# Kernel tuning notes

Hardware: AMD Instinct MI355X
Metric: run time of the kernel (lower is better)

The kernel has to match this reference:

```python
import jax, jax.numpy as jnp
import numpy as np

H = 1024       # hidden_size
VOCAB = 32000  # output_size
L = 128        # max_length
B = 64         # batch


def setup_inputs() -> dict:
    key = jax.random.key(0)
    ks = jax.random.split(key, 16)
    inp = {
        "input_ids": jax.random.randint(ks[0], (1, B), 0, VOCAB),
        "hidden": jax.random.normal(ks[1], (1, B, H), jnp.float32),
        "encoder_outputs": jax.random.normal(ks[2], (L, B, H), jnp.float32),
        # parameters
        "emb": jax.random.normal(ks[3], (VOCAB, H), jnp.float32) * 0.02,
        "attn_W": jax.random.normal(ks[4], (H, 2 * H), jnp.float32) * 0.02,
        "attn_b": jnp.zeros((H,), jnp.float32),
        "v": jax.random.uniform(ks[5], (H,), jnp.float32),
        "w_ih": jax.random.normal(ks[6], (3 * H, 2 * H), jnp.float32) * 0.02,
        "w_hh": jax.random.normal(ks[7], (3 * H, H), jnp.float32) * 0.02,
        "b_ih": jnp.zeros((3 * H,), jnp.float32),
        "b_hh": jnp.zeros((3 * H,), jnp.float32),
        "out_W": jax.random.normal(ks[8], (VOCAB, 3 * H), jnp.float32) * 0.02,
        "out_b": jnp.zeros((VOCAB,), jnp.float32),
    }
    return inp


def reference(input_ids, hidden, encoder_outputs, emb, attn_W, attn_b, v,
              w_ih, w_hh, b_ih, b_hh, out_W, out_b):
    # Dropout in eval mode (identity).
    embedded = emb[input_ids]                      # [1, B, H]
    eo = jnp.transpose(encoder_outputs, (1, 0, 2))  # [B, L, H]
    h0 = hidden[0]                                  # [B, H]

    # Additive (Bahdanau) attention score
    h_rep = jnp.broadcast_to(h0[:, None, :], (eo.shape[0], eo.shape[1], h0.shape[-1]))
    cat = jnp.concatenate([eo, h_rep], axis=-1)     # [B, L, 2H]
    energy = jnp.tanh(jnp.einsum('blk,hk->blh', cat, attn_W) + attn_b)  # [B, L, H]
    scores = jnp.einsum('blh,h->bl', energy, v)     # [B, L]
    attention = jax.nn.softmax(scores, axis=-1)     # [B, L]
    weighted = jnp.einsum('bl,blh->bh', attention, eo)  # [B, H]

    # GRU cell (single layer, single timestep), PyTorch gate order r,z,n
    x = jnp.concatenate([embedded[0], weighted], axis=-1)  # [B, 2H]
    gx = x @ w_ih.T + b_ih                                  # [B, 3H]
    gh = h0 @ w_hh.T + b_hh                                 # [B, 3H]
    xr, xz, xn = jnp.split(gx, 3, axis=-1)
    hr, hz, hn = jnp.split(gh, 3, axis=-1)
    r = jax.nn.sigmoid(xr + hr)
    z = jax.nn.sigmoid(xz + hz)
    n = jnp.tanh(xn + r * hn)
    h_new = (1.0 - z) * n + z * h0                          # [B, H]

    out_cat = jnp.concatenate([h_new, weighted, embedded[0]], axis=-1)  # [B, 3H]
    output = out_cat @ out_W.T + out_b                      # [B, VOCAB]
    return output, h_new[None], attention[:, None, :]
```

## Files before the change

### kernel.cpp

```cpp
#include <hip/hip_runtime.h>
#include <math.h>

#define Hdim 1024
#define VOC 32000
#define LSEQ 128
#define BSZ 64

typedef __attribute__((ext_vector_type(8))) short bf16x8;
typedef __attribute__((ext_vector_type(4))) float f32x4;

__device__ __forceinline__ float fast_tanhf(float x) {
    return 1.0f - 2.0f / (__expf(2.0f * x) + 1.0f);
}
__device__ __forceinline__ float sigmoidf(float x) {
    return 1.0f / (1.0f + __expf(-x));
}
__device__ __forceinline__ short f2bf(float f) {
    unsigned u = __float_as_uint(f);
    unsigned r = (u + 0x7fffu + ((u >> 16) & 1u)) >> 16;
    return (short)r;
}

__device__ __forceinline__ void stage16(const float* __restrict__ src, short* dst) {
    f32x4 v0 = *(const f32x4*)(src);
    f32x4 v1 = *(const f32x4*)(src + 4);
    f32x4 v2 = *(const f32x4*)(src + 8);
    f32x4 v3 = *(const f32x4*)(src + 12);
    bf16x8 p0, p1;
    p0[0] = f2bf(v0[0]); p0[1] = f2bf(v0[1]); p0[2] = f2bf(v0[2]); p0[3] = f2bf(v0[3]);
    p0[4] = f2bf(v1[0]); p0[5] = f2bf(v1[1]); p0[6] = f2bf(v1[2]); p0[7] = f2bf(v1[3]);
    p1[0] = f2bf(v2[0]); p1[1] = f2bf(v2[1]); p1[2] = f2bf(v2[2]); p1[3] = f2bf(v2[3]);
    p1[4] = f2bf(v3[0]); p1[5] = f2bf(v3[1]); p1[6] = f2bf(v3[2]); p1[7] = f2bf(v3[3]);
    *(bf16x8*)(dst) = p0;
    *(bf16x8*)(dst + 8) = p1;
}

__global__ __launch_bounds__(256) void convert_bf16(
    const float* __restrict__ enc, const float* __restrict__ attnW,
    const float* __restrict__ hidden,
    short* __restrict__ enc_bf, short* __restrict__ attnW_bf,
    short* __restrict__ hidden_bf)
{
    const int NG_ENC = (LSEQ * BSZ * Hdim) / 8;
    const int NG_AW  = (Hdim * 2 * Hdim) / 8;
    const int NG_H   = (BSZ * Hdim) / 8;
    const int total = NG_ENC + NG_AW + NG_H;
    for (int g = blockIdx.x * 256 + threadIdx.x; g < total; g += gridDim.x * 256) {
        const float* src; short* dst; int idx;
        if (g < NG_ENC)              { src = enc;    dst = enc_bf;    idx = g; }
        else if (g < NG_ENC + NG_AW) { src = attnW;  dst = attnW_bf;  idx = g - NG_ENC; }
        else                         { src = hidden; dst = hidden_bf; idx = g - NG_ENC - NG_AW; }
        f32x4 a = *(const f32x4*)(src + (size_t)idx * 8);
        f32x4 b = *(const f32x4*)(src + (size_t)idx * 8 + 4);
        bf16x8 p;
        p[0] = f2bf(a[0]); p[1] = f2bf(a[1]); p[2] = f2bf(a[2]); p[3] = f2bf(a[3]);
        p[4] = f2bf(b[0]); p[5] = f2bf(b[1]); p[6] = f2bf(b[2]); p[7] = f2bf(b[3]);
        *(bf16x8*)(dst + (size_t)idx * 8) = p;
    }
}

template<bool BF32>
__global__ __launch_bounds__(256) void gemm256(
    const short* __restrict__ A, int lda,
    const void* __restrict__ Bv, int ldb,
    float* __restrict__ C, int ldc, size_t part_stride, int klen)
{
    __shared__ short As[64 * 72];
    __shared__ short Bs[128 * 72];

    const int t = threadIdx.x;
    const int lane = t & 63, wave = t >> 6;
    const int lr = lane & 15, kh = lane >> 4;
    const int n0 = blockIdx.x * 128;
    const int kstart = blockIdx.y * klen;
    float* Cp = C + (size_t)blockIdx.y * part_stride;

    const int ar = t >> 2, ac = (t & 3) * 16;
    const int br = t >> 1, bc = (t & 1) * 32;

    f32x4 acc[4][2] = {};

    for (int k0 = 0; k0 < klen; k0 += 64) {
        const int kg = kstart + k0;
        {
            const short* s = A + (size_t)ar * lda + kg + ac;
            *(bf16x8*)(As + ar * 72 + ac)     = *(const bf16x8*)(s);
            *(bf16x8*)(As + ar * 72 + ac + 8) = *(const bf16x8*)(s + 8);
        }
        if (!BF32) {
            const short* B = (const short*)Bv;
            const short* s = B + (size_t)(n0 + br) * ldb + kg + bc;
            short* d = Bs + br * 72 + bc;
            *(bf16x8*)(d)      = *(const bf16x8*)(s);
            *(bf16x8*)(d + 8)  = *(const bf16x8*)(s + 8);
            *(bf16x8*)(d + 16) = *(const bf16x8*)(s + 16);
            *(bf16x8*)(d + 24) = *(const bf16x8*)(s + 24);
        } else {
            const float* B = (const float*)Bv;
            const float* s = B + (size_t)(n0 + br) * ldb + kg + bc;
            stage16(s,      Bs + br * 72 + bc);
            stage16(s + 16, Bs + br * 72 + bc + 16);
        }
        __syncthreads();
#pragma unroll
        for (int kk = 0; kk < 64; kk += 32) {
            bf16x8 af[4], bfr[2];
#pragma unroll
            for (int mi = 0; mi < 4; ++mi)
                af[mi] = *(const bf16x8*)(As + (mi * 16 + lr) * 72 + kk + kh * 8);
#pragma unroll
            for (int ni = 0; ni < 2; ++ni)
                bfr[ni] = *(const bf16x8*)(Bs + (wave * 32 + ni * 16 + lr) * 72 + kk + kh * 8);
#pragma unroll
            for (int mi = 0; mi < 4; ++mi)
#pragma unroll
                for (int ni = 0; ni < 2; ++ni)
                    acc[mi][ni] = __builtin_amdgcn_mfma_f32_16x16x32_bf16(
                        af[mi], bfr[ni], acc[mi][ni], 0, 0, 0);
        }
        __syncthreads();
    }

#pragma unroll
    for (int mi = 0; mi < 4; ++mi)
#pragma unroll
        for (int ni = 0; ni < 2; ++ni) {
            const int col = n0 + wave * 32 + ni * 16 + lr;
#pragma unroll
            for (int r = 0; r < 4; ++r) {
                const int row = mi * 16 + kh * 4 + r;
                Cp[(size_t)row * ldc + col] = acc[mi][ni][r];
            }
        }
}

__global__ __launch_bounds__(512) void attn_scores_mfma(
    const short* __restrict__ enc_bf,
    const short* __restrict__ W1_bf,
    const float* __restrict__ u,
    const float* __restrict__ vvec,
    float* __restrict__ scores_part)
{
    __shared__ short As[128 * 72];
    __shared__ short Bs[128 * 72];
    __shared__ float red[8][64];

    const int t = threadIdx.x;
    const int lane = t & 63, wave = t >> 6;
    const int wr = wave >> 2, wc = wave & 3;
    const int lr = lane & 15, kh = lane >> 4;
    const int m0 = blockIdx.x * 128;
    const int n0 = blockIdx.y * 128;

    const int srow = t >> 2, scol = (t & 3) * 16;

    f32x4 acc[4][2] = {};

    for (int kg = 0; kg < Hdim; kg += 64) {
        {
            const short* s = enc_bf + (size_t)(m0 + srow) * Hdim + kg + scol;
            *(bf16x8*)(As + srow * 72 + scol)     = *(const bf16x8*)(s);
            *(bf16x8*)(As + srow * 72 + scol + 8) = *(const bf16x8*)(s + 8);
        }
        {
            const short* s = W1_bf + (size_t)(n0 + srow) * (2 * Hdim) + kg + scol;
            *(bf16x8*)(Bs + srow * 72 + scol)     = *(const bf16x8*)(s);
            *(bf16x8*)(Bs + srow * 72 + scol + 8) = *(const bf16x8*)(s + 8);
        }
        __syncthreads();
#pragma unroll
        for (int kk = 0; kk < 64; kk += 32) {
            bf16x8 af[4], bfr[2];
#pragma unroll
            for (int mi = 0; mi < 4; ++mi)
                af[mi] = *(const bf16x8*)(As + (wr * 64 + mi * 16 + lr) * 72 + kk + kh * 8);
#pragma unroll
            for (int ni = 0; ni < 2; ++ni)
                bfr[ni] = *(const bf16x8*)(Bs + (wc * 32 + ni * 16 + lr) * 72 + kk + kh * 8);
#pragma unroll
            for (int mi = 0; mi < 4; ++mi)
#pragma unroll
                for (int ni = 0; ni < 2; ++ni)
                    acc[mi][ni] = __builtin_amdgcn_mfma_f32_16x16x32_bf16(
                        af[mi], bfr[ni], acc[mi][ni], 0, 0, 0);
        }
        __syncthreads();
    }

    float sv[16];
#pragma unroll
    for (int mi = 0; mi < 4; ++mi)
#pragma unroll
        for (int r = 0; r < 4; ++r) {
            const int lrow = mi * 16 + kh * 4 + r;
            const int b = (wr * 64 + lrow) & 63;
            float s = 0.0f;
#pragma unroll
            for (int ni = 0; ni < 2; ++ni) {
                const int h = n0 + wc * 32 + ni * 16 + lr;
                const float e = fast_tanhf(acc[mi][ni][r] + u[(size_t)b * Hdim + h]);
                s += e * vvec[h];
            }
            sv[mi * 4 + r] = s;
        }
#pragma unroll
    for (int i = 0; i < 16; ++i) {
#pragma unroll
        for (int d = 1; d < 16; d <<= 1)
            sv[i] += __shfl_xor(sv[i], d, 64);
    }
    if (lr == 0) {
#pragma unroll
        for (int mi = 0; mi < 4; ++mi)
#pragma unroll
            for (int r = 0; r < 4; ++r)
                red[wave][mi * 16 + kh * 4 + r] = sv[mi * 4 + r];
    }
    __syncthreads();
    if (t < 128) {
        const int wrr = t >> 6, lrow = t & 63;
        scores_part[(size_t)blockIdx.y * (LSEQ * BSZ) + m0 + t] =
            red[wrr * 4 + 0][lrow] + red[wrr * 4 + 1][lrow] +
            red[wrr * 4 + 2][lrow] + red[wrr * 4 + 3][lrow];
    }
}

__global__ __launch_bounds__(256) void embed_ucomb(
    const float* __restrict__ u4, const float* __restrict__ attnb,
    const int* __restrict__ ids, const float* __restrict__ emb,
    float* __restrict__ u, short* __restrict__ x_bf, short* __restrict__ oc_bf)
{
    const int idx = blockIdx.x * 256 + threadIdx.x;
    if (idx < BSZ * Hdim) {
        u[idx] = u4[idx] + u4[65536 + idx] + u4[2 * 65536 + idx] + u4[3 * 65536 + idx]
               + attnb[idx & 1023];
    } else {
        const int j = idx - BSZ * Hdim;
        const int b = j >> 10, h = j & 1023;
        const short e = f2bf(emb[(size_t)ids[b] * Hdim + h]);
        x_bf[(size_t)b * 2048 + h] = e;
        oc_bf[(size_t)b * 3072 + 2048 + h] = e;
    }
}

__global__ __launch_bounds__(256) void softmax_weighted(
    const float* __restrict__ sp,
    const short* __restrict__ enc_bf,
    float* __restrict__ attn_out,
    short* __restrict__ x_bf,
    short* __restrict__ oc_bf)
{
    const int b = blockIdx.x, t = threadIdx.x;
    __shared__ float aw[LSEQ];
    __shared__ float red[128];

    float s = 0.0f;
    if (t < 128) {
#pragma unroll
        for (int g = 0; g < 8; ++g) s += sp[g * (LSEQ * BSZ) + t * 64 + b];
        red[t] = s;
    }
    __syncthreads();
    for (int off = 64; off > 0; off >>= 1) {
        if (t < off) red[t] = fmaxf(red[t], red[t + off]);
        __syncthreads();
    }
    const float mx = red[0];
    __syncthreads();
    float e = 0.0f;
    if (t < 128) { e = __expf(s - mx); red[t] = e; }
    __syncthreads();
    for (int off = 64; off > 0; off >>= 1) {
        if (t < off) red[t] += red[t + off];
        __syncthreads();
    }
    const float inv = 1.0f / red[0];
    if (t < 128) {
        const float p = e * inv;
        aw[t] = p;
        attn_out[(size_t)b * LSEQ + t] = p;
    }
    __syncthreads();

#pragma unroll
    for (int c = 0; c < 2; ++c) {
        const int h = c * 512 + t * 2;
        float a0 = 0.0f, a1 = 0.0f;
        for (int l = 0; l < LSEQ; ++l) {
            const unsigned w = *(const unsigned*)(enc_bf + ((size_t)l * BSZ + b) * Hdim + h);
            const float p = aw[l];
            a0 = fmaf(p, __uint_as_float(w << 16), a0);
            a1 = fmaf(p, __uint_as_float(w & 0xffff0000u), a1);
        }
        const unsigned packed = (unsigned)(unsigned short)f2bf(a0)
                              | ((unsigned)(unsigned short)f2bf(a1) << 16);
        *(unsigned*)(x_bf + (size_t)b * 2048 + 1024 + h) = packed;
        *(unsigned*)(oc_bf + (size_t)b * 3072 + 1024 + h) = packed;
    }
}

__global__ __launch_bounds__(256) void gru_kernel(
    const float* __restrict__ gx4, const float* __restrict__ gh4,
    const float* __restrict__ b_ih, const float* __restrict__ b_hh,
    const float* __restrict__ h0,
    float* __restrict__ hnew_out, short* __restrict__ oc_bf)
{
    const int idx = blockIdx.x * 256 + threadIdx.x;
    const int b = idx >> 10, h = idx & 1023;
    const size_t g3 = (size_t)b * (3 * Hdim);
    const size_t P = (size_t)BSZ * 3 * Hdim;
    float xr = b_ih[h], xz = b_ih[Hdim + h], xn = b_ih[2 * Hdim + h];
    float hr = b_hh[h], hz = b_hh[Hdim + h], hn = b_hh[2 * Hdim + h];
#pragma unroll
    for (int s = 0; s < 4; ++s) {
        xr += gx4[s * P + g3 + h];
        xz += gx4[s * P + g3 + Hdim + h];
        xn += gx4[s * P + g3 + 2 * Hdim + h];
        hr += gh4[s * P + g3 + h];
        hz += gh4[s * P + g3 + Hdim + h];
        hn += gh4[s * P + g3 + 2 * Hdim + h];
    }
    const float r = sigmoidf(xr + hr);
    const float z = sigmoidf(xz + hz);
    const float n = fast_tanhf(xn + r * hn);
    const float hv = (1.0f - z) * n + z * h0[(size_t)b * Hdim + h];
    hnew_out[(size_t)b * Hdim + h] = hv;
    oc_bf[g3 + h] = f2bf(hv);
}

__global__ __launch_bounds__(512) void outproj512(
    const short* __restrict__ A,
    const float* __restrict__ B,
    float* __restrict__ Cpart,
    int klen)
{
    __shared__ short As[64 * 72];
    __shared__ short Bs[128 * 72];

    const int t = threadIdx.x;
    const int lane = t & 63, wave = t >> 6;
    const int lr = lane & 15, kh = lane >> 4;
    const int n0 = blockIdx.x * 128;
    const int kstart = blockIdx.y * klen;
    float* Cp = Cpart + (size_t)blockIdx.y * (64 * VOC);

    const int ar = t >> 3, ac = (t & 7) * 8;
    const int br = t >> 2, bc = (t & 3) * 16;

    f32x4 acc[4] = {};

    for (int k0 = 0; k0 < klen; k0 += 64) {
        const int kg = kstart + k0;
        *(bf16x8*)(As + ar * 72 + ac) =
            *(const bf16x8*)(A + (size_t)ar * 3072 + kg + ac);
        stage16(B + (size_t)(n0 + br) * 3072 + kg + bc, Bs + br * 72 + bc);
        __syncthreads();
#pragma unroll
        for (int kk = 0; kk < 64; kk += 32) {
            bf16x8 af[4], bfr;
#pragma unroll
            for (int mi = 0; mi < 4; ++mi)
                af[mi] = *(const bf16x8*)(As + (mi * 16 + lr) * 72 + kk + kh * 8);
            bfr = *(const bf16x8*)(Bs + (wave * 16 + lr) * 72 + kk + kh * 8);
#pragma unroll
            for (int mi = 0; mi < 4; ++mi)
                acc[mi] = __builtin_amdgcn_mfma_f32_16x16x32_bf16(af[mi], bfr, acc[mi], 0, 0, 0);
        }
        __syncthreads();
    }

    const int col = n0 + wave * 16 + lr;
#pragma unroll
    for (int mi = 0; mi < 4; ++mi)
#pragma unroll
        for (int r = 0; r < 4; ++r) {
            const int row = mi * 16 + kh * 4 + r;
            Cp[(size_t)row * VOC + col] = acc[mi][r];
        }
}

__global__ __launch_bounds__(256) void oproj_comb(
    const float* __restrict__ part, const float* __restrict__ out_b,
    float* __restrict__ logits)
{
    const size_t i4 = ((size_t)blockIdx.x * 256 + threadIdx.x) * 4;
    f32x4 a = *(const f32x4*)(part + i4);
    f32x4 b = *(const f32x4*)(part + (size_t)64 * VOC + i4);
    const int col = (int)(i4 % VOC);
    f32x4 bb = *(const f32x4*)(out_b + col);
    f32x4 o = a + b + bb;
    *(f32x4*)(logits + i4) = o;
}

extern "C" void kernel_launch(void* const* d_in, const int* in_sizes, int n_in,
                              void* d_out, int out_size, void* d_ws, size_t ws_size,
                              hipStream_t stream)
{
    const int*   ids    = (const int*)d_in[0];
    const float* hidden = (const float*)d_in[1];
    const float* enc    = (const float*)d_in[2];
    const float* emb    = (const float*)d_in[3];
    const float* attnW  = (const float*)d_in[4];
    const float* attnb  = (const float*)d_in[5];
    const float* vvec   = (const float*)d_in[6];
    const float* w_ih   = (const float*)d_in[7];
    const float* w_hh   = (const float*)d_in[8];
    const float* b_ih   = (const float*)d_in[9];
    const float* b_hh   = (const float*)d_in[10];
    const float* out_W  = (const float*)d_in[11];
    const float* out_b  = (const float*)d_in[12];

    float* out        = (float*)d_out;
    float* out_logits = out;
    float* out_hnew   = out + (size_t)BSZ * VOC;
    float* out_attn   = out_hnew + (size_t)BSZ * Hdim;

    float* ws = (float*)d_ws;
    short* enc_bf    = (short*)ws;
    short* attnW_bf  = (short*)(ws + 4194304);
    short* hidden_bf = (short*)(ws + 4194304 + 1048576);
    float* ws_u4  = ws + 4194304 + 1048576 + 32768;
    float* ws_u   = ws_u4 + 262144;
    float* ws_sp  = ws_u + 65536;
    short* x_bf   = (short*)(ws_sp + 65536);
    short* oc_bf  = (short*)(ws_sp + 65536 + 65536);
    float* ws_gx4 = ws_sp + 65536 + 65536 + 98304;
    float* ws_gh4 = ws_gx4 + 786432;
    float* ws_op  = ws_gh4 + 786432;

    convert_bf16<<<dim3(1024), 256, 0, stream>>>(
        enc, attnW, hidden, enc_bf, attnW_bf, hidden_bf);

    gemm256<false><<<dim3(Hdim / 128, 4), 256, 0, stream>>>(
        hidden_bf, Hdim, attnW_bf + Hdim, 2 * Hdim,
        ws_u4, Hdim, (size_t)BSZ * Hdim, 256);

    embed_ucomb<<<dim3(2 * BSZ * Hdim / 256), 256, 0, stream>>>(
        ws_u4, attnb, ids, emb, ws_u, x_bf, oc_bf);

    attn_scores_mfma<<<dim3(LSEQ / 2, 8), 512, 0, stream>>>(
        enc_bf, attnW_bf, ws_u, vvec, ws_sp);

    softmax_weighted<<<dim3(BSZ), 256, 0, stream>>>(
        ws_sp, enc_bf, out_attn, x_bf, oc_bf);

    gemm256<true><<<dim3(3 * Hdim / 128, 4), 256, 0, stream>>>(
        x_bf, 2 * Hdim, w_ih, 2 * Hdim,
        ws_gx4, 3 * Hdim, (size_t)BSZ * 3 * Hdim, 512);
    gemm256<true><<<dim3(3 * Hdim / 128, 4), 256, 0, stream>>>(
        hidden_bf, Hdim, w_hh, Hdim,
        ws_gh4, 3 * Hdim, (size_t)BSZ * 3 * Hdim, 256);

    gru_kernel<<<dim3(BSZ * Hdim / 256), 256, 0, stream>>>(
        ws_gx4, ws_gh4, b_ih, b_hh, hidden, out_hnew, oc_bf);

    outproj512<<<dim3(VOC / 128, 2), 512, 0, stream>>>(
        oc_bf, out_W, ws_op, 1536);
    oproj_comb<<<dim3(BSZ * VOC / 4 / 256), 256, 0, stream>>>(
        ws_op, out_b, out_logits);
}
```

Measured before the change: 191.5 us.

## Fuse split-K combines and small kernels to cut launches and partial buffers

Removes the output-projection split-K and its combine kernel: each block now covers the full K and adds the bias in its epilogue. This avoids writing and re-reading the partial logits. The u-combine kernel is folded into the attention-score kernel, which reduces u4 plus the bias into LDS for each block. The embedding gather moves into the softmax kernel, and the gx and gh GEMMs are merged into one launch. In exchange, the attention kernel does redundant u reductions and uses more LDS, which may lower occupancy, and the output projection has less K-parallelism per block.

Result: no change. 190.0 us (-0.8%).

```diff
diff --git a/kernel.cpp b/kernel.cpp
--- a/kernel.cpp
+++ b/kernel.cpp
@@ -59,11 +59,10 @@
     }
 }
 
-template<bool BF32>
-__global__ __launch_bounds__(256) void gemm256(
-    const short* __restrict__ A, int lda,
-    const void* __restrict__ Bv, int ldb,
-    float* __restrict__ C, int ldc, size_t part_stride, int klen)
+__global__ __launch_bounds__(256) void ugemm(
+    const short* __restrict__ A,
+    const short* __restrict__ B,
+    float* __restrict__ C)
 {
     __shared__ short As[64 * 72];
     __shared__ short Bs[128 * 72];
@@ -72,34 +71,28 @@
     const int lane = t & 63, wave = t >> 6;
     const int lr = lane & 15, kh = lane >> 4;
     const int n0 = blockIdx.x * 128;
-    const int kstart = blockIdx.y * klen;
-    float* Cp = C + (size_t)blockIdx.y * part_stride;
+    const int kstart = blockIdx.y * 256;
+    float* Cp = C + (size_t)blockIdx.y * (BSZ * Hdim);
 
     const int ar = t >> 2, ac = (t & 3) * 16;
     const int br = t >> 1, bc = (t & 1) * 32;
 
     f32x4 acc[4][2] = {};
 
-    for (int k0 = 0; k0 < klen; k0 += 64) {
+    for (int k0 = 0; k0 < 256; k0 += 64) {
         const int kg = kstart + k0;
         {
-            const short* s = A + (size_t)ar * lda + kg + ac;
+            const short* s = A + (size_t)ar * Hdim + kg + ac;
             *(bf16x8*)(As + ar * 72 + ac)     = *(const bf16x8*)(s);
             *(bf16x8*)(As + ar * 72 + ac + 8) = *(const bf16x8*)(s + 8);
         }
-        if (!BF32) {
-            const short* B = (const short*)Bv;
-            const short* s = B + (size_t)(n0 + br) * ldb + kg + bc;
+        {
+            const short* s = B + (size_t)(n0 + br) * (2 * Hdim) + kg + bc;
             short* d = Bs + br * 72 + bc;
             *(bf16x8*)(d)      = *(const bf16x8*)(s);
             *(bf16x8*)(d + 8)  = *(const bf16x8*)(s + 8);
             *(bf16x8*)(d + 16) = *(const bf16x8*)(s + 16);
             *(bf16x8*)(d + 24) = *(const bf16x8*)(s + 24);
-        } else {
-            const float* B = (const float*)Bv;
-            const float* s = B + (size_t)(n0 + br) * ldb + kg + bc;
-            stage16(s,      Bs + br * 72 + bc);
-            stage16(s + 16, Bs + br * 72 + bc + 16);
         }
         __syncthreads();
 #pragma unroll
@@ -129,7 +122,7 @@
 #pragma unroll
             for (int r = 0; r < 4; ++r) {
                 const int row = mi * 16 + kh * 4 + r;
-                Cp[(size_t)row * ldc + col] = acc[mi][ni][r];
+                Cp[(size_t)row * Hdim + col] = acc[mi][ni][r];
             }
         }
 }
@@ -137,13 +130,15 @@
 __global__ __launch_bounds__(512) void attn_scores_mfma(
     const short* __restrict__ enc_bf,
     const short* __restrict__ W1_bf,
-    const float* __restrict__ u,
+    const float* __restrict__ u4,
+    const float* __restrict__ attnb,
     const float* __restrict__ vvec,
     float* __restrict__ scores_part)
 {
     __shared__ short As[128 * 72];
     __shared__ short Bs[128 * 72];
     __shared__ float red[8][64];
+    __shared__ float u_lds[64 * 128];
 
     const int t = threadIdx.x;
     const int lane = t & 63, wave = t >> 6;
@@ -154,6 +149,13 @@
 
     const int srow = t >> 2, scol = (t & 3) * 16;
 
+    for (int i = t; i < 64 * 128; i += 512) {
+        const int b = i >> 7, hl = i & 127;
+        const size_t g = (size_t)b * Hdim + n0 + hl;
+        u_lds[i] = u4[g] + u4[65536 + g] + u4[2 * 65536 + g] + u4[3 * 65536 + g]
+                 + attnb[n0 + hl];
+    }
+
     f32x4 acc[4][2] = {};
 
     for (int kg = 0; kg < Hdim; kg += 64) {
@@ -193,13 +195,13 @@
 #pragma unroll
         for (int r = 0; r < 4; ++r) {
             const int lrow = mi * 16 + kh * 4 + r;
-            const int b = (wr * 64 + lrow) & 63;
+            const int b = lrow;
             float s = 0.0f;
 #pragma unroll
             for (int ni = 0; ni < 2; ++ni) {
-                const int h = n0 + wc * 32 + ni * 16 + lr;
-                const float e = fast_tanhf(acc[mi][ni][r] + u[(size_t)b * Hdim + h]);
-                s += e * vvec[h];
+                const int hl = wc * 32 + ni * 16 + lr;
+                const float e = fast_tanhf(acc[mi][ni][r] + u_lds[b * 128 + hl]);
+                s += e * vvec[n0 + hl];
             }
             sv[mi * 4 + r] = s;
         }
@@ -225,27 +227,11 @@
     }
 }
 
-__global__ __launch_bounds__(256) void embed_ucomb(
-    const float* __restrict__ u4, const float* __restrict__ attnb,
-    const int* __restrict__ ids, const float* __restrict__ emb,
-    float* __restrict__ u, short* __restrict__ x_bf, short* __restrict__ oc_bf)
-{
-    const int idx = blockIdx.x * 256 + threadIdx.x;
-    if (idx < BSZ * Hdim) {
-        u[idx] = u4[idx] + u4[65536 + idx] + u4[2 * 65536 + idx] + u4[3 * 65536 + idx]
-               + attnb[idx & 1023];
-    } else {
-        const int j = idx - BSZ * Hdim;
-        const int b = j >> 10, h = j & 1023;
-        const short e = f2bf(emb[(size_t)ids[b] * Hdim + h]);
-        x_bf[(size_t)b * 2048 + h] = e;
-        oc_bf[(size_t)b * 3072 + 2048 + h] = e;
-    }
-}
-
 __global__ __launch_bounds__(256) void softmax_weighted(
     const float* __restrict__ sp,
     const short* __restrict__ enc_bf,
+    const int* __restrict__ ids,
+    const float* __restrict__ emb,
     float* __restrict__ attn_out,
     short* __restrict__ x_bf,
     short* __restrict__ oc_bf)
@@ -253,6 +239,17 @@
     const int b = blockIdx.x, t = threadIdx.x;
     __shared__ float aw[LSEQ];
     __shared__ float red[128];
+
+    {
+        const int id = ids[b];
+#pragma unroll
+        for (int i = 0; i < 4; ++i) {
+            const int h = t * 4 + i;
+            const short e = f2bf(emb[(size_t)id * Hdim + h]);
+            x_bf[(size_t)b * 2048 + h] = e;
+            oc_bf[(size_t)b * 3072 + 2048 + h] = e;
+        }
+    }
 
     float s = 0.0f;
     if (t < 128) {
@@ -299,6 +296,77 @@
     }
 }
 
+__global__ __launch_bounds__(256) void gxgh_gemm(
+    const short* __restrict__ x_bf, const float* __restrict__ w_ih,
+    const short* __restrict__ hidden_bf, const float* __restrict__ w_hh,
+    float* __restrict__ gx4, float* __restrict__ gh4)
+{
+    __shared__ short As[64 * 72];
+    __shared__ short Bs[128 * 72];
+
+    const int t = threadIdx.x;
+    const int lane = t & 63, wave = t >> 6;
+    const int lr = lane & 15, kh = lane >> 4;
+
+    const short* A; const float* B; float* C; int lda, klen, n0;
+    if (blockIdx.x < 24) {
+        A = x_bf; B = w_ih; C = gx4; lda = 2048; klen = 512; n0 = blockIdx.x * 128;
+    } else {
+        A = hidden_bf; B = w_hh; C = gh4; lda = 1024; klen = 256; n0 = (blockIdx.x - 24) * 128;
+    }
+    const int kstart = blockIdx.y * klen;
+    float* Cp = C + (size_t)blockIdx.y * (BSZ * 3 * Hdim);
+
+    const int ar = t >> 2, ac = (t & 3) * 16;
+    const int br = t >> 1, bc = (t & 1) * 32;
+
+    f32x4 acc[4][2] = {};
+
+    for (int k0 = 0; k0 < klen; k0 += 64) {
+        const int kg = kstart + k0;
+        {
+            const short* s = A + (size_t)ar * lda + kg + ac;
+            *(bf16x8*)(As + ar * 72 + ac)     = *(const bf16x8*)(s);
+            *(bf16x8*)(As + ar * 72 + ac + 8) = *(const bf16x8*)(s + 8);
+        }
+        {
+            const float* s = B + (size_t)(n0 + br) * lda + kg + bc;
+            stage16(s,      Bs + br * 72 + bc);
+            stage16(s + 16, Bs + br * 72 + bc + 16);
+        }
+        __syncthreads();
+#pragma unroll
+        for (int kk = 0; kk < 64; kk += 32) {
+            bf16x8 af[4], bfr[2];
+#pragma unroll
+            for (int mi = 0; mi < 4; ++mi)
+                af[mi] = *(const bf16x8*)(As + (mi * 16 + lr) * 72 + kk + kh * 8);
+#pragma unroll
+            for (int ni = 0; ni < 2; ++ni)
+                bfr[ni] = *(const bf16x8*)(Bs + (wave * 32 + ni * 16 + lr) * 72 + kk + kh * 8);
+#pragma unroll
+            for (int mi = 0; mi < 4; ++mi)
+#pragma unroll
+                for (int ni = 0; ni < 2; ++ni)
+                    acc[mi][ni] = __builtin_amdgcn_mfma_f32_16x16x32_bf16(
+                        af[mi], bfr[ni], acc[mi][ni], 0, 0, 0);
+        }
+        __syncthreads();
+    }
+
+#pragma unroll
+    for (int mi = 0; mi < 4; ++mi)
+#pragma unroll
+        for (int ni = 0; ni < 2; ++ni) {
+            const int col = n0 + wave * 32 + ni * 16 + lr;
+#pragma unroll
+            for (int r = 0; r < 4; ++r) {
+                const int row = mi * 16 + kh * 4 + r;
+                Cp[(size_t)row * (3 * Hdim) + col] = acc[mi][ni][r];
+            }
+        }
+}
+
 __global__ __launch_bounds__(256) void gru_kernel(
     const float* __restrict__ gx4, const float* __restrict__ gh4,
     const float* __restrict__ b_ih, const float* __restrict__ b_hh,
@@ -328,32 +396,30 @@
     oc_bf[g3 + h] = f2bf(hv);
 }
 
-__global__ __launch_bounds__(512) void outproj512(
+__global__ __launch_bounds__(256) void outproj_direct(
     const short* __restrict__ A,
     const float* __restrict__ B,
-    float* __restrict__ Cpart,
-    int klen)
+    const float* __restrict__ bias,
+    float* __restrict__ logits)
 {
     __shared__ short As[64 * 72];
-    __shared__ short Bs[128 * 72];
+    __shared__ short Bs[64 * 72];
 
     const int t = threadIdx.x;
     const int lane = t & 63, wave = t >> 6;
     const int lr = lane & 15, kh = lane >> 4;
-    const int n0 = blockIdx.x * 128;
-    const int kstart = blockIdx.y * klen;
-    float* Cp = Cpart + (size_t)blockIdx.y * (64 * VOC);
-
-    const int ar = t >> 3, ac = (t & 7) * 8;
-    const int br = t >> 2, bc = (t & 3) * 16;
+    const int n0 = blockIdx.x * 64;
+    const int sr = t >> 2, sc = (t & 3) * 16;
 
     f32x4 acc[4] = {};
 
-    for (int k0 = 0; k0 < klen; k0 += 64) {
-        const int kg = kstart + k0;
-        *(bf16x8*)(As + ar * 72 + ac) =
-            *(const bf16x8*)(A + (size_t)ar * 3072 + kg + ac);
-        stage16(B + (size_t)(n0 + br) * 3072 + kg + bc, Bs + br * 72 + bc);
+    for (int kg = 0; kg < 3072; kg += 64) {
+        {
+            const short* s = A + (size_t)sr * 3072 + kg + sc;
+            *(bf16x8*)(As + sr * 72 + sc)     = *(const bf16x8*)(s);
+            *(bf16x8*)(As + sr * 72 + sc + 8) = *(const bf16x8*)(s + 8);
+        }
+        stage16(B + (size_t)(n0 + sr) * 3072 + kg + sc, Bs + sr * 72 + sc);
         __syncthreads();
 #pragma unroll
         for (int kk = 0; kk < 64; kk += 32) {
@@ -370,26 +436,14 @@
     }
 
     const int col = n0 + wave * 16 + lr;
+    const float bb = bias[col];
 #pragma unroll
     for (int mi = 0; mi < 4; ++mi)
 #pragma unroll
         for (int r = 0; r < 4; ++r) {
             const int row = mi * 16 + kh * 4 + r;
-            Cp[(size_t)row * VOC + col] = acc[mi][r];
-        }
-}
-
-__global__ __launch_bounds__(256) void oproj_comb(
-    const float* __restrict__ part, const float* __restrict__ out_b,
-    float* __restrict__ logits)
-{
-    const size_t i4 = ((size_t)blockIdx.x * 256 + threadIdx.x) * 4;
-    f32x4 a = *(const f32x4*)(part + i4);
-    f32x4 b = *(const f32x4*)(part + (size_t)64 * VOC + i4);
-    const int col = (int)(i4 % VOC);
-    f32x4 bb = *(const f32x4*)(out_b + col);
-    f32x4 o = a + b + bb;
-    *(f32x4*)(logits + i4) = o;
+            logits[(size_t)row * VOC + col] = acc[mi][r] + bb;
+        }
 }
 
 extern "C" void kernel_launch(void* const* d_in, const int* in_sizes, int n_in,
@@ -418,44 +472,32 @@
     float* ws = (float*)d_ws;
     short* enc_bf    = (short*)ws;
     short* attnW_bf  = (short*)(ws + 4194304);
-    short* hidden_bf = (short*)(ws + 4194304 + 1048576);
-    float* ws_u4  = ws + 4194304 + 1048576 + 32768;
-    float* ws_u   = ws_u4 + 262144;
-    float* ws_sp  = ws_u + 65536;
+    short* hidden_bf = (short*)(ws + 5242880);
+    float* ws_u4  = ws + 5275648;
+    float* ws_sp  = ws_u4 + 262144;
     short* x_bf   = (short*)(ws_sp + 65536);
-    short* oc_bf  = (short*)(ws_sp + 65536 + 65536);
-    float* ws_gx4 = ws_sp + 65536 + 65536 + 98304;
+    short* oc_bf  = (short*)(ws_sp + 131072);
+    float* ws_gx4 = ws_sp + 229376;
     float* ws_gh4 = ws_gx4 + 786432;
-    float* ws_op  = ws_gh4 + 786432;
 
     convert_bf16<<<dim3(1024), 256, 0, stream>>>(
         enc, attnW, hidden, enc_bf, attnW_bf, hidden_bf);
 
-    gemm256<false><<<dim3(Hdim / 128, 4), 256, 0, stream>>>(
-        hidden_bf, Hdim, attnW_bf + Hdim, 2 * Hdim,
-        ws_u4, Hdim, (size_t)BSZ * Hdim, 256);
-
-    embed_ucomb<<<dim3(2 * BSZ * Hdim / 256), 256, 0, stream>>>(
-        ws_u4, attnb, ids, emb, ws_u, x_bf, oc_bf);
+    ugemm<<<dim3(Hdim / 128, 4), 256, 0, stream>>>(
+        hidden_bf, attnW_bf + Hdim, ws_u4);
 
     attn_scores_mfma<<<dim3(LSEQ / 2, 8), 512, 0, stream>>>(
-        enc_bf, attnW_bf, ws_u, vvec, ws_sp);
+        enc_bf, attnW_bf, ws_u4, attnb, vvec, ws_sp);
 
     softmax_weighted<<<dim3(BSZ), 256, 0, stream>>>(
-        ws_sp, enc_bf, out_attn, x_bf, oc_bf);
-
-    gemm256<true><<<dim3(3 * Hdim / 128, 4), 256, 0, stream>>>(
-        x_bf, 2 * Hdim, w_ih, 2 * Hdim,
-        ws_gx4, 3 * Hdim, (size_t)BSZ * 3 * Hdim, 512);
-    gemm256<true><<<dim3(3 * Hdim / 128, 4), 256, 0, stream>>>(
-        hidden_bf, Hdim, w_hh, Hdim,
-        ws_gh4, 3 * Hdim, (size_t)BSZ * 3 * Hdim, 256);
+        ws_sp, enc_bf, ids, emb, out_attn, x_bf, oc_bf);
+
+    gxgh_gemm<<<dim3(48, 4), 256, 0, stream>>>(
+        x_bf, w_ih, hidden_bf, w_hh, ws_gx4, ws_gh4);
 
     gru_kernel<<<dim3(BSZ * Hdim / 256), 256, 0, stream>>>(
         ws_gx4, ws_gh4, b_ih, b_hh, hidden, out_hnew, oc_bf);
 
-    outproj512<<<dim3(VOC / 128, 2), 512, 0, stream>>>(
-        oc_bf, out_W, ws_op, 1536);
-    oproj_comb<<<dim3(BSZ * VOC / 4 / 256), 256, 0, stream>>>(
-        ws_op, out_b, out_logits);
-}
+    outproj_direct<<<dim3(VOC / 64), 256, 0, stream>>>(
+        oc_bf, out_W, out_b, out_logits);
+}
```
